# Performance work log

Measured on AMD Instinct MI355X. Metric: run time of the kernel, lower is better.

Reference implementation:

```python
import jax, jax.numpy as jnp
import numpy as np

N_NODES = 100_000
N_EDGES = 2_500_000
HID = 32
SE3_NORM = 1.0 / np.sqrt(32.0)  # e3nn path normalization for 32x0e -> 32x0e


def setup_inputs() -> dict:
    key = jax.random.key(0)
    ks = jax.random.split(key, 14)
    inp = {
        "pos": jax.random.normal(ks[0], (N_NODES, 3), dtype=jnp.float32),
        "edge_index": jax.random.randint(ks[1], (2, N_EDGES), 0, N_NODES, dtype=jnp.int64),
        "Wl1": jax.random.normal(ks[2], (2, HID), dtype=jnp.float32) * 0.5,
        "bl1": jax.random.normal(ks[3], (HID,), dtype=jnp.float32) * 0.1,
        "Wr1": jax.random.normal(ks[4], (2, HID), dtype=jnp.float32) * 0.5,
        "Wl2": jax.random.normal(ks[5], (HID, HID), dtype=jnp.float32) * 0.15,
        "bl2": jax.random.normal(ks[6], (HID,), dtype=jnp.float32) * 0.1,
        "Wr2": jax.random.normal(ks[7], (HID, HID), dtype=jnp.float32) * 0.15,
        "Wse1": jax.random.normal(ks[8], (HID, HID), dtype=jnp.float32) * 0.15,
        "Wse2": jax.random.normal(ks[9], (HID, HID), dtype=jnp.float32) * 0.15,
        "W3": jax.random.normal(ks[10], (HID, HID), dtype=jnp.float32) * 0.15,
        "b3": jax.random.normal(ks[11], (HID,), dtype=jnp.float32) * 0.1,
        "W4": jax.random.normal(ks[12], (HID, 1), dtype=jnp.float32) * 0.15,
        "b4": jax.random.normal(ks[13], (1,), dtype=jnp.float32) * 0.1,
        "alpha": jnp.float32(0.5),
    }
    return inp


def _sage_conv(x, src, dst, Wl, bl, Wr, n_nodes):
    # gather messages from source nodes, scatter-sum onto destination nodes
    agg = jax.ops.segment_sum(x[src], dst, num_segments=n_nodes)  # [N, d_in]
    return agg @ Wl + bl + x @ Wr  # lin_l(agg) + lin_r(x); lin_r has no bias


def reference(pos, edge_index, Wl1, bl1, Wr1, Wl2, bl2, Wr2, Wse1, Wse2, W3, b3, W4, b4, alpha):
    n = pos.shape[0]
    x = pos[:, :2]                       # [N, 2]
    src, dst = edge_index[0], edge_index[1]

    h1 = _sage_conv(x, src, dst, Wl1, bl1, Wr1, n)   # [N, 32]
    h1 = jax.nn.leaky_relu(h1, negative_slope=0.01)  # dropout = identity (eval)
    h1 = (h1 @ Wse1) * SE3_NORM                      # SE3Linear 32x0e->32x0e

    h2 = _sage_conv(h1, src, dst, Wl2, bl2, Wr2, n)
    h2 = jax.nn.leaky_relu(h2, negative_slope=0.01)
    h2 = (h2 @ Wse2) * SE3_NORM

    x_skip = alpha * h1 + h2
    x_out = jax.nn.relu(x_skip @ W3 + b3)            # mlp3 (dropout identity)
    pred = x_out @ W4 + b4                           # mlp4
    return pred.squeeze(-1)                          # [N]
```

## Files before the change

kernel.cpp:

```cpp
#include <hip/hip_runtime.h>
#include <hip/hip_fp16.h>

#define HID 32
#define LEAKY 0.01f
#define SE3NORM 0.17677669529663687f
#define SCAN_TILE 1024
#define NBK 128
#define GA 1024
#define CHCAP 8192
#define NPB2 64


__global__ void k_bhist(const int* __restrict__ ei, int* __restrict__ bh,
                        int E, int B1, int chunk) {
    extern __shared__ int lh[];
    int g = blockIdx.x;
    for (int i = threadIdx.x; i < B1; i += 256) lh[i] = 0;
    __syncthreads();
    int beg = g * chunk, end = min(E, beg + chunk);
    for (int e = beg + (int)threadIdx.x; e < end; e += 256)
        atomicAdd(&lh[ei[E + e] >> 7], 1);
    __syncthreads();
    for (int b = threadIdx.x; b < B1; b += 256) bh[b * GA + g] = lh[b];
}

__global__ void k_scan1(int* __restrict__ data, int* __restrict__ bsum, int M) {
    __shared__ int lds[256];
    int t = threadIdx.x;
    int base = blockIdx.x * SCAN_TILE + t * 4;
    int v0 = (base + 0 < M) ? data[base + 0] : 0;
    int v1 = (base + 1 < M) ? data[base + 1] : 0;
    int v2 = (base + 2 < M) ? data[base + 2] : 0;
    int v3 = (base + 3 < M) ? data[base + 3] : 0;
    int s = v0 + v1 + v2 + v3;
    lds[t] = s;
    __syncthreads();
    for (int off = 1; off < 256; off <<= 1) {
        int x = (t >= off) ? lds[t - off] : 0;
        __syncthreads();
        lds[t] += x;
        __syncthreads();
    }
    int ex = lds[t] - s;
    if (base + 0 < M) data[base + 0] = ex;
    if (base + 1 < M) data[base + 1] = ex + v0;
    if (base + 2 < M) data[base + 2] = ex + v0 + v1;
    if (base + 3 < M) data[base + 3] = ex + v0 + v1 + v2;
    if (t == 255) bsum[blockIdx.x] = lds[255];
}

__global__ void k_scan2(int* __restrict__ bsum, int B) {
    __shared__ int lds[256];
    int t = threadIdx.x;
    int k0 = t * 4;
    int v0 = (k0 + 0 < B) ? bsum[k0 + 0] : 0;
    int v1 = (k0 + 1 < B) ? bsum[k0 + 1] : 0;
    int v2 = (k0 + 2 < B) ? bsum[k0 + 2] : 0;
    int v3 = (k0 + 3 < B) ? bsum[k0 + 3] : 0;
    int s = v0 + v1 + v2 + v3;
    lds[t] = s;
    __syncthreads();
    for (int off = 1; off < 256; off <<= 1) {
        int x = (t >= off) ? lds[t - off] : 0;
        __syncthreads();
        lds[t] += x;
        __syncthreads();
    }
    int ex = lds[t] - s;
    if (k0 + 0 < B) { bsum[k0 + 0] = ex; ex += v0; }
    if (k0 + 1 < B) { bsum[k0 + 1] = ex; ex += v1; }
    if (k0 + 2 < B) { bsum[k0 + 2] = ex; ex += v2; }
    if (k0 + 3 < B) { bsum[k0 + 3] = ex; ex += v3; }
}

__global__ void k_scan3(int* __restrict__ data, const int* __restrict__ bsum,
                        int* __restrict__ cursor, int M, int N) {
    int i = blockIdx.x * blockDim.x + threadIdx.x;
    if (i >= M) return;
    int off = data[i] + bsum[i / SCAN_TILE];
    data[i] = off;
    if (cursor && i < N) cursor[i] = off;
}

__global__ __launch_bounds__(256, 1) void k_bscatter2(
        const int* __restrict__ ei, const int* __restrict__ bh,
        const int* __restrict__ bsum,
        int* __restrict__ bucketed, int E, int B1, int chunk) {
    extern __shared__ int lh[];
    int* cur  = lh;
    int* hist = lh + B1;
    int* base = lh + 2 * B1;
    unsigned short* perm = (unsigned short*)(lh + 3 * B1);
    __shared__ int scanbuf[256];
    const int g = blockIdx.x;
    const int t = threadIdx.x;
    const int beg = g * chunk;
    const int end = min(E, beg + chunk);
    const int sz = end - beg;

    for (int b = t; b < B1; b += 256) {
        int idx = b * GA + g;
        cur[b] = bh[idx] + bsum[idx >> 10];
        hist[b] = 0;
    }
    __syncthreads();
    for (int i = t; i < sz; i += 256)
        atomicAdd(&hist[ei[E + beg + i] >> 7], 1);
    __syncthreads();
    {
        int k0 = t * 4;
        int c0 = (k0 + 0 < B1) ? hist[k0 + 0] : 0;
        int c1 = (k0 + 1 < B1) ? hist[k0 + 1] : 0;
        int c2 = (k0 + 2 < B1) ? hist[k0 + 2] : 0;
        int c3 = (k0 + 3 < B1) ? hist[k0 + 3] : 0;
        int ssum = c0 + c1 + c2 + c3;
        scanbuf[t] = ssum;
        __syncthreads();
        for (int off = 1; off < 256; off <<= 1) {
            int x = (t >= off) ? scanbuf[t - off] : 0;
            __syncthreads();
            scanbuf[t] += x;
            __syncthreads();
        }
        int ex = scanbuf[t] - ssum;
        if (k0 + 0 < B1) { base[k0 + 0] = ex; ex += c0; }
        if (k0 + 1 < B1) { base[k0 + 1] = ex; ex += c1; }
        if (k0 + 2 < B1) { base[k0 + 2] = ex; ex += c2; }
        if (k0 + 3 < B1) { base[k0 + 3] = ex; ex += c3; }
    }
    __syncthreads();
    for (int b = t; b < B1; b += 256) hist[b] = base[b];
    __syncthreads();
    for (int i = t; i < sz; i += 256) {
        int bid = ei[E + beg + i] >> 7;
        int p = atomicAdd(&hist[bid], 1);
        perm[p] = (unsigned short)i;
    }
    __syncthreads();
    for (int p = t; p < sz; p += 256) {
        int i = perm[p];
        int d = ei[E + beg + i];
        int s = ei[beg + i];
        int bid = d >> 7;
        bucketed[cur[bid] + (p - base[bid])] = s | ((d & (NBK - 1)) << 24);
    }
}

__global__ __launch_bounds__(512, 1) void k_bsort(
        const int* __restrict__ bh, const int* __restrict__ bsum,
        const int* __restrict__ bucketed,
        int* __restrict__ sorted_src, int* __restrict__ offsets,
        int E, int N, int B1) {
    __shared__ int hist[NBK], sc[NBK], base[NBK];
    __shared__ unsigned short perm[CHCAP];
    int b = blockIdx.x;
    int t = threadIdx.x;
    int i0 = b * GA;
    int bs = bh[i0] + bsum[i0 >> 10];
    int be;
    if (b == B1 - 1) be = E;
    else { int i1 = (b + 1) * GA; be = bh[i1] + bsum[i1 >> 10]; }
    int sz = be - bs;
    if (t < NBK) hist[t] = 0;
    __syncthreads();

    if (sz <= CHCAP) {
        for (int i = t; i < sz; i += 512)
            atomicAdd(&hist[bucketed[bs + i] >> 24], 1);
        __syncthreads();
        int v = (t < NBK) ? hist[t] : 0;
        if (t < NBK) sc[t] = v;
        __syncthreads();
        for (int off = 1; off < NBK; off <<= 1) {
            int x = (t < NBK && t >= off) ? sc[t - off] : 0;
            __syncthreads();
            if (t < NBK) sc[t] += x;
            __syncthreads();
        }
        if (t < NBK) base[t] = sc[t] - v;
        __syncthreads();
        if (t < NBK) hist[t] = base[t];
        __syncthreads();
        for (int i = t; i < sz; i += 512) {
            int p = atomicAdd(&hist[bucketed[bs + i] >> 24], 1);
            perm[p] = (unsigned short)i;
        }
        __syncthreads();
        for (int p = t; p < sz; p += 512)
            sorted_src[bs + p] = bucketed[bs + perm[p]] & 0x00FFFFFF;
    } else {
        for (int e = bs + t; e < be; e += 512)
            atomicAdd(&hist[bucketed[e] >> 24], 1);
        __syncthreads();
        int v = (t < NBK) ? hist[t] : 0;
        if (t < NBK) sc[t] = v;
        __syncthreads();
        for (int off = 1; off < NBK; off <<= 1) {
            int x = (t < NBK && t >= off) ? sc[t - off] : 0;
            __syncthreads();
            if (t < NBK) sc[t] += x;
            __syncthreads();
        }
        if (t < NBK) base[t] = sc[t] - v;
        __syncthreads();
        if (t < NBK) hist[t] = base[t];
        __syncthreads();
        for (int e = bs + t; e < be; e += 512) {
            int pv = bucketed[e];
            int p = atomicAdd(&hist[pv >> 24], 1);
            sorted_src[bs + p] = pv & 0x00FFFFFF;
        }
    }
    int node = b * NBK + t;
    if (t < NBK && node < N) offsets[node] = bs + base[t];
    if (b == B1 - 1 && t == 0) offsets[N] = E;
}

__global__ void k_hist_rank(const int* __restrict__ ei, int* __restrict__ hist,
                            int* __restrict__ rank, int E) {
    int base = (blockIdx.x * blockDim.x + threadIdx.x) * 4;
#pragma unroll
    for (int u = 0; u < 4; u++) {
        int e = base + u;
        if (e < E) rank[e] = atomicAdd(&hist[ei[E + e]], 1);
    }
}
__global__ void k_hist(const int* __restrict__ ei, int* __restrict__ hist, int E) {
    int base = (blockIdx.x * blockDim.x + threadIdx.x) * 4;
#pragma unroll
    for (int u = 0; u < 4; u++) {
        int e = base + u;
        if (e < E) atomicAdd(&hist[ei[E + e]], 1);
    }
}
__global__ void k_scatter_rank(const int* __restrict__ ei, const int* __restrict__ offsets,
                               const int* __restrict__ rank, int* __restrict__ sorted_src, int E) {
    int base = (blockIdx.x * blockDim.x + threadIdx.x) * 4;
#pragma unroll
    for (int u = 0; u < 4; u++) {
        int e = base + u;
        if (e < E) sorted_src[offsets[ei[E + e]] + rank[e]] = ei[e];
    }
}
__global__ void k_scatter_atomic(const int* __restrict__ ei, int* __restrict__ cursor,
                                 int* __restrict__ sorted_src, int E) {
    int base = (blockIdx.x * blockDim.x + threadIdx.x) * 4;
#pragma unroll
    for (int u = 0; u < 4; u++) {
        int e = base + u;
        if (e < E) {
            int p = atomicAdd(&cursor[ei[E + e]], 1);
            sorted_src[p] = ei[e];
        }
    }
}

__global__ __launch_bounds__(256, 1) void k_node1(
                        const int* __restrict__ offsets, const int* __restrict__ sorted_src,
                        const float* __restrict__ pos,
                        const float* __restrict__ Wl1, const float* __restrict__ bl1,
                        const float* __restrict__ Wr1, const float* __restrict__ Wse1,
                        __half* __restrict__ h1, int N) {
    __shared__ float sWl1[2 * HID], sWr1[2 * HID], sbl1[HID], sWse1[HID * HID];
    __shared__ float sH[32][HID + 4];
    for (int i = threadIdx.x; i < 2 * HID; i += blockDim.x) { sWl1[i] = Wl1[i]; sWr1[i] = Wr1[i]; }
    for (int i = threadIdx.x; i < HID; i += blockDim.x) sbl1[i] = bl1[i];
    for (int i = threadIdx.x; i < HID * HID; i += blockDim.x) sWse1[i] = Wse1[i];
    __syncthreads();

    const int lt = threadIdx.x;
    const int nodeL = lt >> 3;
    const int t = lt & 7;
    const int node = blockIdx.x * 32 + nodeL;
    const bool live = node < N;

    float a0 = 0.f, a1 = 0.f;
    if (live) {
        int beg = offsets[node], end = offsets[node + 1];
        for (int e = beg + t; e < end; e += 8) {
            int s = sorted_src[e];
            a0 += pos[s * 3];
            a1 += pos[s * 3 + 1];
        }
    }
    a0 += __shfl_xor(a0, 1); a1 += __shfl_xor(a1, 1);
    a0 += __shfl_xor(a0, 2); a1 += __shfl_xor(a1, 2);
    a0 += __shfl_xor(a0, 4); a1 += __shfl_xor(a1, 4);

    if (live) {
        float x0 = pos[3 * node], x1 = pos[3 * node + 1];
#pragma unroll
        for (int jj = 0; jj < 4; jj++) {
            int k = t * 4 + jj;
            float v = a0 * sWl1[k] + a1 * sWl1[HID + k] + sbl1[k] + x0 * sWr1[k] + x1 * sWr1[HID + k];
            sH[nodeL][k] = v > 0.f ? v : LEAKY * v;
        }
    }
    __syncthreads();

    if (live) {
        float4 acc = make_float4(0.f, 0.f, 0.f, 0.f);
#pragma unroll 8
        for (int k = 0; k < HID; k++) {
            float hk = sH[nodeL][k];
            float4 w = *(const float4*)&sWse1[k * HID + t * 4];
            acc.x += hk * w.x; acc.y += hk * w.y;
            acc.z += hk * w.z; acc.w += hk * w.w;
        }
        union Pack4 { __half h[4]; float2 v; } p;
        p.h[0] = __float2half(acc.x * SE3NORM);
        p.h[1] = __float2half(acc.y * SE3NORM);
        p.h[2] = __float2half(acc.z * SE3NORM);
        p.h[3] = __float2half(acc.w * SE3NORM);
        *(float2*)&h1[(size_t)node * HID + t * 4] = p.v;
    }
}

__device__ __forceinline__ void acc_h1frag(float2 r, float4& acc) {
    __half2 p01 = __builtin_bit_cast(__half2, r.x);
    __half2 p23 = __builtin_bit_cast(__half2, r.y);
    acc.x += __low2float(p01); acc.y += __high2float(p01);
    acc.z += __low2float(p23); acc.w += __high2float(p23);
}

__global__ __launch_bounds__(512, 1) void k_node2out(
                           const int* __restrict__ offsets, const int* __restrict__ sorted_src,
                           const __half* __restrict__ h1,
                           const float* __restrict__ Wl2, const float* __restrict__ bl2,
                           const float* __restrict__ Wr2, const float* __restrict__ Wse2,
                           const float* __restrict__ W3, const float* __restrict__ b3,
                           const float* __restrict__ W4, const float* __restrict__ b4,
                           const float* __restrict__ alpha_p,
                           float* __restrict__ out, int N) {
    __shared__ float sWl2[HID * HID], sWr2[HID * HID], sWse2[HID * HID], sW3[HID * HID];
    __shared__ float sbl2[HID], sb3[HID], sW4[HID];
    __shared__ float sb4, salpha;
    __shared__ float sA[NPB2][HID + 4], sB[NPB2][HID + 4];
    for (int i = threadIdx.x; i < HID * HID; i += blockDim.x) {
        sWl2[i] = Wl2[i]; sWr2[i] = Wr2[i]; sWse2[i] = Wse2[i]; sW3[i] = W3[i];
    }
    for (int i = threadIdx.x; i < HID; i += blockDim.x) { sbl2[i] = bl2[i]; sb3[i] = b3[i]; sW4[i] = W4[i]; }
    if (threadIdx.x == 0) { sb4 = b4[0]; salpha = alpha_p[0]; }
    __syncthreads();

    const int lt = threadIdx.x;
    const int nodeL = lt >> 3;
    const int t = lt & 7;
    const int node = blockIdx.x * NPB2 + nodeL;
    const bool live = node < N;

    if (live) {
        float2 ro = *(const float2*)&h1[(size_t)node * HID + t * 4];

        int beg = offsets[node], end = offsets[node + 1];
        float4 acc = make_float4(0.f, 0.f, 0.f, 0.f);
        int e = beg;
        for (; e + 8 <= end; e += 8) {
            int s0 = __builtin_nontemporal_load(&sorted_src[e + 0]);
            int s1 = __builtin_nontemporal_load(&sorted_src[e + 1]);
            int s2 = __builtin_nontemporal_load(&sorted_src[e + 2]);
            int s3 = __builtin_nontemporal_load(&sorted_src[e + 3]);
            int s4 = __builtin_nontemporal_load(&sorted_src[e + 4]);
            int s5 = __builtin_nontemporal_load(&sorted_src[e + 5]);
            int s6 = __builtin_nontemporal_load(&sorted_src[e + 6]);
            int s7 = __builtin_nontemporal_load(&sorted_src[e + 7]);
            float2 r0 = *(const float2*)&h1[(size_t)s0 * HID + t * 4];
            float2 r1 = *(const float2*)&h1[(size_t)s1 * HID + t * 4];
            float2 r2 = *(const float2*)&h1[(size_t)s2 * HID + t * 4];
            float2 r3 = *(const float2*)&h1[(size_t)s3 * HID + t * 4];
            float2 r4 = *(const float2*)&h1[(size_t)s4 * HID + t * 4];
            float2 r5 = *(const float2*)&h1[(size_t)s5 * HID + t * 4];
            float2 r6 = *(const float2*)&h1[(size_t)s6 * HID + t * 4];
            float2 r7 = *(const float2*)&h1[(size_t)s7 * HID + t * 4];
            acc_h1frag(r0, acc); acc_h1frag(r1, acc);
            acc_h1frag(r2, acc); acc_h1frag(r3, acc);
            acc_h1frag(r4, acc); acc_h1frag(r5, acc);
            acc_h1frag(r6, acc); acc_h1frag(r7, acc);
        }
        for (; e < end; e++) {
            int s = __builtin_nontemporal_load(&sorted_src[e]);
            float2 r = *(const float2*)&h1[(size_t)s * HID + t * 4];
            acc_h1frag(r, acc);
        }
        __half2 o01 = __builtin_bit_cast(__half2, ro.x);
        __half2 o23 = __builtin_bit_cast(__half2, ro.y);
        float4 own = make_float4(__low2float(o01), __high2float(o01),
                                 __low2float(o23), __high2float(o23));
        *(float4*)&sA[nodeL][t * 4] = acc;
        *(float4*)&sB[nodeL][t * 4] = own;
    }
    __syncthreads();

    float h2r[4];
    if (live) {
        h2r[0] = sbl2[t * 4 + 0]; h2r[1] = sbl2[t * 4 + 1];
        h2r[2] = sbl2[t * 4 + 2]; h2r[3] = sbl2[t * 4 + 3];
#pragma unroll 8
        for (int k = 0; k < HID; k++) {
            float a = sA[nodeL][k];
            float b = sB[nodeL][k];
            float4 wl = *(const float4*)&sWl2[k * HID + t * 4];
            float4 wr = *(const float4*)&sWr2[k * HID + t * 4];
            h2r[0] += a * wl.x + b * wr.x;
            h2r[1] += a * wl.y + b * wr.y;
            h2r[2] += a * wl.z + b * wr.z;
            h2r[3] += a * wl.w + b * wr.w;
        }
#pragma unroll
        for (int jj = 0; jj < 4; jj++) h2r[jj] = h2r[jj] > 0.f ? h2r[jj] : LEAKY * h2r[jj];
    }
    __syncthreads();
    if (live) {
        float4 st = make_float4(h2r[0], h2r[1], h2r[2], h2r[3]);
        *(float4*)&sA[nodeL][t * 4] = st;
    }
    __syncthreads();

    if (live) {
        float4 acc = make_float4(0.f, 0.f, 0.f, 0.f);
#pragma unroll 8
        for (int k = 0; k < HID; k++) {
            float a = sA[nodeL][k];
            float4 w = *(const float4*)&sWse2[k * HID + t * 4];
            acc.x += a * w.x; acc.y += a * w.y;
            acc.z += a * w.z; acc.w += a * w.w;
        }
        float4 own = *(const float4*)&sB[nodeL][t * 4];
        own.x = salpha * own.x + acc.x * SE3NORM;
        own.y = salpha * own.y + acc.y * SE3NORM;
        own.z = salpha * own.z + acc.z * SE3NORM;
        own.w = salpha * own.w + acc.w * SE3NORM;
        *(float4*)&sB[nodeL][t * 4] = own;
    }
    __syncthreads();

    float acc4[4];
    acc4[0] = sb3[t * 4 + 0]; acc4[1] = sb3[t * 4 + 1];
    acc4[2] = sb3[t * 4 + 2]; acc4[3] = sb3[t * 4 + 3];
    if (live) {
#pragma unroll 8
        for (int k = 0; k < HID; k++) {
            float s = sB[nodeL][k];
            float4 w = *(const float4*)&sW3[k * HID + t * 4];
            acc4[0] += s * w.x; acc4[1] += s * w.y;
            acc4[2] += s * w.z; acc4[3] += s * w.w;
        }
    }
    float part = 0.f;
#pragma unroll
    for (int jj = 0; jj < 4; jj++)
        part += (acc4[jj] > 0.f ? acc4[jj] : 0.f) * sW4[t * 4 + jj];
    part += __shfl_xor(part, 1);
    part += __shfl_xor(part, 2);
    part += __shfl_xor(part, 4);
    if (live && t == 0) out[node] = part + sb4;
}

extern "C" void kernel_launch(void* const* d_in, const int* in_sizes, int n_in,
                              void* d_out, int out_size, void* d_ws, size_t ws_size,
                              hipStream_t stream) {
    const float* pos  = (const float*)d_in[0];
    const int*   ei   = (const int*)d_in[1];
    const float* Wl1  = (const float*)d_in[2];
    const float* bl1  = (const float*)d_in[3];
    const float* Wr1  = (const float*)d_in[4];
    const float* Wl2  = (const float*)d_in[5];
    const float* bl2  = (const float*)d_in[6];
    const float* Wr2  = (const float*)d_in[7];
    const float* Wse1 = (const float*)d_in[8];
    const float* Wse2 = (const float*)d_in[9];
    const float* W3   = (const float*)d_in[10];
    const float* b3   = (const float*)d_in[11];
    const float* W4   = (const float*)d_in[12];
    const float* b4   = (const float*)d_in[13];
    const float* alp  = (const float*)d_in[14];
    float* out = (float*)d_out;

    const int N = in_sizes[0] / 3;
    const int E = in_sizes[1] / 2;
    const int blk = 256;
    const size_t h1bytes = (size_t)N * HID * sizeof(__half);

    const int B1 = (N + NBK - 1) / NBK;
    const int M2 = B1 * GA;
    const int S2 = (M2 + SCAN_TILE - 1) / SCAN_TILE;
    {
        int* bh         = (int*)d_ws;
        int* bsum       = bh + M2;
        int* bucketed   = bsum + 1024;
        int* sorted_src = bucketed + E;
        int* offsets    = sorted_src + E;
        uintptr_t hp = ((uintptr_t)(offsets + N + 1) + 15) & ~(uintptr_t)15;
        size_t need = (hp - (uintptr_t)d_ws) + h1bytes;
        const int chunk = (E + GA - 1) / GA;
        if (need <= ws_size && S2 <= 1024 && B1 <= 1024 && chunk <= CHCAP) {
            __half* h1 = (__half*)hp;
            const size_t ldsB = (size_t)B1 * sizeof(int);
            const size_t ldsB2 = (size_t)(3 * B1) * sizeof(int) + (size_t)CHCAP * sizeof(unsigned short);
            k_bhist<<<GA, 256, ldsB, stream>>>(ei, bh, E, B1, chunk);
            k_scan1<<<S2, 256, 0, stream>>>(bh, bsum, M2);
            k_scan2<<<1, 256, 0, stream>>>(bsum, S2);
            k_bscatter2<<<GA, 256, ldsB2, stream>>>(ei, bh, bsum, bucketed, E, B1, chunk);
            k_bsort<<<B1, 512, 0, stream>>>(bh, bsum, bucketed, sorted_src, offsets, E, N, B1);
            k_node1<<<(N + 31) / 32, 256, 0, stream>>>(offsets, sorted_src, pos,
                                                       Wl1, bl1, Wr1, Wse1, h1, N);
            k_node2out<<<(N + NPB2 - 1) / NPB2, 512, 0, stream>>>(offsets, sorted_src, h1,
                                                          Wl2, bl2, Wr2, Wse2,
                                                          W3, b3, W4, b4, alp, out, N);
            return;
        }
    }

    const int M = N + 1;
    const int B = (M + SCAN_TILE - 1) / SCAN_TILE;
    int* hist       = (int*)d_ws;
    int* offsets    = hist + M;
    int* bsum       = offsets + M;
    int* sorted_src = bsum + 1024;
    int* aux        = sorted_src + E;
    uintptr_t hpA = ((uintptr_t)(aux + E) + 15) & ~(uintptr_t)15;
    uintptr_t hpB = ((uintptr_t)(aux + N) + 15) & ~(uintptr_t)15;
    size_t needA = (hpA - (uintptr_t)d_ws) + h1bytes;
    const bool useRank = (needA <= ws_size);
    __half* h1 = (__half*)(useRank ? hpA : hpB);

    hipMemsetAsync(hist, 0, (size_t)M * sizeof(int), stream);
    const int egrid4 = (E / 4 + blk) / blk;
    if (useRank) {
        k_hist_rank<<<egrid4, blk, 0, stream>>>(ei, hist, aux, E);
    } else {
        k_hist<<<egrid4, blk, 0, stream>>>(ei, hist, E);
    }
    k_scan1<<<B, 256, 0, stream>>>(hist, bsum, M);
    k_scan2<<<1, 256, 0, stream>>>(bsum, B);
    k_scan3<<<(M + blk - 1) / blk, blk, 0, stream>>>(hist, bsum, useRank ? nullptr : aux, M, N);
    int* offs = hist;
    if (useRank) {
        k_scatter_rank<<<egrid4, blk, 0, stream>>>(ei, offs, aux, sorted_src, E);
    } else {
        k_scatter_atomic<<<egrid4, blk, 0, stream>>>(ei, aux, sorted_src, E);
    }
    k_node1<<<(N + 31) / 32, 256, 0, stream>>>(offs, sorted_src, pos, Wl1, bl1, Wr1, Wse1, h1, N);
    k_node2out<<<(N + NPB2 - 1) / NPB2, 512, 0, stream>>>(offs, sorted_src, h1, Wl2, bl2, Wr2, Wse2,
                                                  W3, b3, W4, b4, alp, out, N);
}
```

Baseline: 241.3 us.

## Fuse layer-1 node aggregation and SE3 linear into the bucket sort kernel

Merges the first SAGE layer node kernel into the per-bucket sort kernel. Each block has just written sorted sources for its 128 destination nodes, so it aggregates neighbour positions, applies lin_l/lin_r, leaky ReLU and the Wse1 projection, and writes h1 as fp16. This removes one kernel launch and the re-read of offsets and sorted_src, and the sorted_src reads may hit in cache. In exchange the sort kernel uses more LDS and registers and runs only B1 (~782) blocks at 1 per CU, so the gather of pos has less parallelism than the separate kernel had.

```diff
diff --git a/kernel.cpp b/kernel.cpp
--- a/kernel.cpp
+++ b/kernel.cpp
@@ -146,15 +146,25 @@
     }
 }
 
-__global__ __launch_bounds__(512, 1) void k_bsort(
+__global__ __launch_bounds__(512, 1) void k_bsortn1(
         const int* __restrict__ bh, const int* __restrict__ bsum,
         const int* __restrict__ bucketed,
+        const float* __restrict__ pos,
+        const float* __restrict__ Wl1, const float* __restrict__ bl1,
+        const float* __restrict__ Wr1, const float* __restrict__ Wse1,
         int* __restrict__ sorted_src, int* __restrict__ offsets,
-        int E, int N, int B1) {
+        __half* __restrict__ h1, int E, int N, int B1) {
     __shared__ int hist[NBK], sc[NBK], base[NBK];
     __shared__ unsigned short perm[CHCAP];
+    __shared__ float aggx[NBK], aggy[NBK];
+    __shared__ float sWl1[2 * HID], sWr1[2 * HID], sbl1[HID], sWse1[HID * HID];
+    __shared__ float sH[64][HID + 4];
     int b = blockIdx.x;
     int t = threadIdx.x;
+    for (int i = t; i < 2 * HID; i += 512) { sWl1[i] = Wl1[i]; sWr1[i] = Wr1[i]; }
+    for (int i = t; i < HID; i += 512) sbl1[i] = bl1[i];
+    for (int i = t; i < HID * HID; i += 512) sWse1[i] = Wse1[i];
+
     int i0 = b * GA;
     int bs = bh[i0] + bsum[i0 >> 10];
     int be;
@@ -211,9 +221,65 @@
             sorted_src[bs + p] = pv & 0x00FFFFFF;
         }
     }
-    int node = b * NBK + t;
-    if (t < NBK && node < N) offsets[node] = bs + base[t];
+    int nodeg = b * NBK + t;
+    if (t < NBK && nodeg < N) offsets[nodeg] = bs + base[t];
     if (b == B1 - 1 && t == 0) offsets[N] = E;
+
+    __syncthreads();
+
+    {
+        const int dl = t >> 2;
+        const int lane = t & 3;
+        const int sbeg = bs + base[dl];
+        const int cnt = hist[dl] - base[dl];
+        float a0 = 0.f, a1 = 0.f;
+        for (int i = lane; i < cnt; i += 4) {
+            int s = sorted_src[sbeg + i];
+            a0 += pos[s * 3];
+            a1 += pos[s * 3 + 1];
+        }
+        a0 += __shfl_xor(a0, 1); a1 += __shfl_xor(a1, 1);
+        a0 += __shfl_xor(a0, 2); a1 += __shfl_xor(a1, 2);
+        if (lane == 0) { aggx[dl] = a0; aggy[dl] = a1; }
+    }
+    __syncthreads();
+
+    const int nodeL = t >> 3;
+    const int tt = t & 7;
+    for (int c = 0; c < 2; c++) {
+        const int dl = c * 64 + nodeL;
+        const int node = b * NBK + dl;
+        const bool live = node < N;
+        if (live) {
+            float a0 = aggx[dl], a1 = aggy[dl];
+            float x0 = pos[3 * node], x1 = pos[3 * node + 1];
+#pragma unroll
+            for (int jj = 0; jj < 4; jj++) {
+                int k = tt * 4 + jj;
+                float v = a0 * sWl1[k] + a1 * sWl1[HID + k] + sbl1[k]
+                        + x0 * sWr1[k] + x1 * sWr1[HID + k];
+                sH[nodeL][k] = v > 0.f ? v : LEAKY * v;
+            }
+        }
+        __syncthreads();
+        if (live) {
+            float4 acc = make_float4(0.f, 0.f, 0.f, 0.f);
+#pragma unroll 8
+            for (int k = 0; k < HID; k++) {
+                float hk = sH[nodeL][k];
+                float4 w = *(const float4*)&sWse1[k * HID + tt * 4];
+                acc.x += hk * w.x; acc.y += hk * w.y;
+                acc.z += hk * w.z; acc.w += hk * w.w;
+            }
+            union Pack4 { __half h[4]; float2 v; } p;
+            p.h[0] = __float2half(acc.x * SE3NORM);
+            p.h[1] = __float2half(acc.y * SE3NORM);
+            p.h[2] = __float2half(acc.z * SE3NORM);
+            p.h[3] = __float2half(acc.w * SE3NORM);
+            *(float2*)&h1[(size_t)node * HID + tt * 4] = p.v;
+        }
+        __syncthreads();
+    }
 }
 
 __global__ void k_hist_rank(const int* __restrict__ ei, int* __restrict__ hist,
@@ -501,9 +567,9 @@
             k_scan1<<<S2, 256, 0, stream>>>(bh, bsum, M2);
             k_scan2<<<1, 256, 0, stream>>>(bsum, S2);
             k_bscatter2<<<GA, 256, ldsB2, stream>>>(ei, bh, bsum, bucketed, E, B1, chunk);
-            k_bsort<<<B1, 512, 0, stream>>>(bh, bsum, bucketed, sorted_src, offsets, E, N, B1);
-            k_node1<<<(N + 31) / 32, 256, 0, stream>>>(offsets, sorted_src, pos,
-                                                       Wl1, bl1, Wr1, Wse1, h1, N);
+            k_bsortn1<<<B1, 512, 0, stream>>>(bh, bsum, bucketed, pos,
+                                              Wl1, bl1, Wr1, Wse1,
+                                              sorted_src, offsets, h1, E, N, B1);
             k_node2out<<<(N + NPB2 - 1) / NPB2, 512, 0, stream>>>(offsets, sorted_src, h1,
                                                           Wl2, bl2, Wr2, Wse2,
                                                           W3, b3, W4, b4, alp, out, N);
```

Measured after the change: 238.3 us, median of 2. No clear change (-1.2%).
